# Kernel tuning notes

Hardware: AMD Instinct MI355X
Metric: run time of the kernel (lower is better)

Reference implementation:

```python
import jax, jax.numpy as jnp
import numpy as np

NUM_LAYERS = 2
FEATURES = 128
INPUT_SIZE = 128
HIDDEN = 512
BATCH = 128
SEQ_LEN = 512
PRED_LEN = 128


def _uniform(key, shape, fan):
    bound = 1.0 / np.sqrt(fan)
    return jax.random.uniform(key, shape, jnp.float32, -bound, bound)


def setup_inputs() -> dict:
    key = jax.random.key(0)
    ks = jax.random.split(key, 14)
    inp = {}
    inp["x"] = jax.random.normal(ks[0], (BATCH, SEQ_LEN, FEATURES), jnp.float32)
    # encoder Linear(features -> input_size)
    inp["enc_w"] = _uniform(ks[1], (INPUT_SIZE, FEATURES), FEATURES)
    inp["enc_b"] = _uniform(ks[2], (INPUT_SIZE,), FEATURES)
    # decoder Linear(hidden -> input_size)
    inp["dec_w"] = _uniform(ks[3], (INPUT_SIZE, HIDDEN), HIDDEN)
    inp["dec_b"] = _uniform(ks[4], (INPUT_SIZE,), HIDDEN)
    # LSTM layer 0 (input_size -> hidden), gate order i,f,g,o as in PyTorch
    inp["wih0"] = _uniform(ks[5], (4 * HIDDEN, INPUT_SIZE), HIDDEN)
    inp["whh0"] = _uniform(ks[6], (4 * HIDDEN, HIDDEN), HIDDEN)
    inp["bih0"] = _uniform(ks[7], (4 * HIDDEN,), HIDDEN)
    inp["bhh0"] = _uniform(ks[8], (4 * HIDDEN,), HIDDEN)
    # LSTM layer 1 (hidden -> hidden)
    inp["wih1"] = _uniform(ks[9], (4 * HIDDEN, HIDDEN), HIDDEN)
    inp["whh1"] = _uniform(ks[10], (4 * HIDDEN, HIDDEN), HIDDEN)
    inp["bih1"] = _uniform(ks[11], (4 * HIDDEN,), HIDDEN)
    inp["bhh1"] = _uniform(ks[12], (4 * HIDDEN,), HIDDEN)
    inp["pred_len"] = PRED_LEN
    return inp


def _lstm_cell(h, c, inp, wih, whh, bih, bhh):
    g = inp @ wih.T + bih + h @ whh.T + bhh  # [B, 4H]
    i, f, gg, o = jnp.split(g, 4, axis=-1)
    c = jax.nn.sigmoid(f) * c + jax.nn.sigmoid(i) * jnp.tanh(gg)
    h = jax.nn.sigmoid(o) * jnp.tanh(c)
    return h, c


def reference(x, enc_w, enc_b, dec_w, dec_b, wih0, whh0, bih0, bhh0,
              wih1, whh1, bih1, bhh1, pred_len):
    B, S, Fdim = x.shape
    T = S + pred_len - 1
    # pad x to T steps; beyond S the input comes from the previous output
    x_pad = jnp.concatenate([x, jnp.zeros((B, pred_len - 1, Fdim), x.dtype)], axis=1)
    x_t = jnp.transpose(x_pad, (1, 0, 2))  # [T, B, F]

    def step(carry, xs):
        h0, c0, h1, c1, prev_out = carry
        xt, t = xs
        inp = jnp.where(t < S, xt, prev_out)
        e = inp @ enc_w.T + enc_b                    # encoder
        h0, c0 = _lstm_cell(h0, c0, e, wih0, whh0, bih0, bhh0)
        h1, c1 = _lstm_cell(h1, c1, h0, wih1, whh1, bih1, bhh1)
        out = h1 @ dec_w.T + dec_b                   # decoder
        return (h0, c0, h1, c1, out), out

    z = jnp.zeros((B, HIDDEN), x.dtype)
    init = (z, z, z, z, jnp.zeros((B, Fdim), x.dtype))
    _, outs = jax.lax.scan(step, init, (x_t, jnp.arange(T)))
    # keep steps idx >= S-1 (pred_len outputs), back to [B, pred_len, input_size]
    return jnp.transpose(outs[S - 1:], (1, 0, 2))
```

## Files before the change

### kernel.cpp

```cpp
#include <hip/hip_runtime.h>
#include <math.h>

#define HID 512
#define FEAT 128
#define SEQL 512
#define PREDL 128
#define NWG 256
#define HK 516
#define EK 132

typedef float v2f __attribute__((ext_vector_type(2)));

__device__ __forceinline__ float sigf_(float x) { return 1.0f / (1.0f + __expf(-x)); }
__device__ __forceinline__ float tanh_(float x) {
  float ax = fabsf(x);
  float e2 = __expf(-2.0f * ax);
  return copysignf((1.0f - e2) / (1.0f + e2), x);
}
__device__ __forceinline__ v2f mkv2(float a, float b) { v2f r; r[0] = a; r[1] = b; return r; }

__device__ __forceinline__ void stg_sc(float* p, float v) {
  __hip_atomic_store(p, v, __ATOMIC_RELAXED, __HIP_MEMORY_SCOPE_AGENT);
}

__device__ __forceinline__ void bar_arrive(int* __restrict__ bar, int grp,
                                           int phase, int tid, bool& last) {
  __syncthreads();
  if (tid == 0) {
    const int a = __hip_atomic_fetch_add(bar + grp * 32, 1, __ATOMIC_RELAXED,
                                         __HIP_MEMORY_SCOPE_AGENT);
    last = (a == 32 * phase - 1);
    if (last)
      __hip_atomic_store(bar + 512 + grp * 32, phase, __ATOMIC_RELAXED,
                         __HIP_MEMORY_SCOPE_AGENT);
  }
  asm volatile("" ::: "memory");
}
__device__ __forceinline__ void bar_wait(int* __restrict__ bar, int grp,
                                         int phase, int tid, bool last) {
  asm volatile("" ::: "memory");
  if (tid == 0 && !last) {
    while (__hip_atomic_load(bar + 512 + grp * 32, __ATOMIC_RELAXED,
                             __HIP_MEMORY_SCOPE_AGENT) < phase)
      __builtin_amdgcn_s_sleep(1);
  }
  __syncthreads();
}

__device__ __forceinline__ void stage4(float* __restrict__ dst,
                                       const float* __restrict__ src,
                                       int b0, int lane512) {
  const int kb = lane512 >> 2;
  const int bq = (lane512 & 3) * 4;
  const float* p0 = src + (size_t)kb * 128 + b0 + bq;
  const float* p1 = src + ((size_t)kb + 128) * 128 + b0 + bq;
  const float* p2 = src + ((size_t)kb + 256) * 128 + b0 + bq;
  const float* p3 = src + ((size_t)kb + 384) * 128 + b0 + bq;
  float4 r0, r1, r2, r3;
  asm volatile(
      "global_load_dwordx4 %0, %4, off sc0 sc1\n\t"
      "global_load_dwordx4 %1, %5, off sc0 sc1\n\t"
      "global_load_dwordx4 %2, %6, off sc0 sc1\n\t"
      "global_load_dwordx4 %3, %7, off sc0 sc1\n\t"
      "s_waitcnt vmcnt(0)"
      : "=&v"(r0), "=&v"(r1), "=&v"(r2), "=&v"(r3)
      : "v"(p0), "v"(p1), "v"(p2), "v"(p3)
      : "memory");
  dst[(bq + 0) * HK + kb] = r0.x; dst[(bq + 1) * HK + kb] = r0.y;
  dst[(bq + 2) * HK + kb] = r0.z; dst[(bq + 3) * HK + kb] = r0.w;
  dst[(bq + 0) * HK + kb + 128] = r1.x; dst[(bq + 1) * HK + kb + 128] = r1.y;
  dst[(bq + 2) * HK + kb + 128] = r1.z; dst[(bq + 3) * HK + kb + 128] = r1.w;
  dst[(bq + 0) * HK + kb + 256] = r2.x; dst[(bq + 1) * HK + kb + 256] = r2.y;
  dst[(bq + 2) * HK + kb + 256] = r2.z; dst[(bq + 3) * HK + kb + 256] = r2.w;
  dst[(bq + 0) * HK + kb + 384] = r3.x; dst[(bq + 1) * HK + kb + 384] = r3.y;
  dst[(bq + 2) * HK + kb + 384] = r3.z; dst[(bq + 3) * HK + kb + 384] = r3.w;
}
__device__ __forceinline__ void stage_x1(float* __restrict__ dst,
                                         const float* __restrict__ x, int t,
                                         int b0, int lane512) {
  const int bb = lane512 >> 5;
  const int fq = (lane512 & 31) * 4;
  const float4 v =
      *(const float4*)(x + ((size_t)(b0 + bb) * SEQL + t) * FEAT + fq);
  *(float4*)(dst + bb * EK + fq) = v;
}

__device__ __forceinline__ void pkf(v2f& a01, v2f& a23, float4 w, float h) {
  v2f hh; hh[0] = h; hh[1] = h;
  v2f lo; lo[0] = w.x; lo[1] = w.y;
  v2f hi; hi[0] = w.z; hi[1] = w.w;
  a01 = __builtin_elementwise_fma(lo, hh, a01);
  a23 = __builtin_elementwise_fma(hi, hh, a23);
}
__device__ __forceinline__ void gemv_fused8(v2f& a01, v2f& a23,
                                            const float4* __restrict__ W8,
                                            size_t base,
                                            const float* __restrict__ rA,
                                            const float* __restrict__ rB,
                                            int k4b, int k4e) {
#pragma unroll 2
  for (int k4 = k4b; k4 < k4e; ++k4) {
    const float4 hA = *(const float4*)(rA + k4 * 4);
    const float4 hB = *(const float4*)(rB + k4 * 4);
    const size_t o = base + (size_t)k4 * 8;
    pkf(a01, a23, W8[o + 0], hA.x); pkf(a01, a23, W8[o + 1], hB.x);
    pkf(a01, a23, W8[o + 2], hA.y); pkf(a01, a23, W8[o + 3], hB.y);
    pkf(a01, a23, W8[o + 4], hA.z); pkf(a01, a23, W8[o + 5], hB.z);
    pkf(a01, a23, W8[o + 6], hA.w); pkf(a01, a23, W8[o + 7], hB.w);
  }
}
__device__ __forceinline__ void gemv_half8(v2f& a01, v2f& a23,
                                           const float4* __restrict__ W8,
                                           size_t base, int sel,
                                           const float* __restrict__ row,
                                           int k4b, int k4e) {
#pragma unroll 4
  for (int k4 = k4b; k4 < k4e; ++k4) {
    const float4 h = *(const float4*)(row + k4 * 4);
    const size_t o = base + (size_t)k4 * 8 + sel;
    pkf(a01, a23, W8[o + 0], h.x);
    pkf(a01, a23, W8[o + 2], h.y);
    pkf(a01, a23, W8[o + 4], h.z);
    pkf(a01, a23, W8[o + 6], h.w);
  }
}
__device__ __forceinline__ void gemv_p4(v2f& a01, v2f& a23,
                                        const float4* __restrict__ W4,
                                        size_t base,
                                        const float* __restrict__ row,
                                        int k4b, int k4e) {
#pragma unroll 4
  for (int k4 = k4b; k4 < k4e; ++k4) {
    const float4 h = *(const float4*)(row + k4 * 4);
    const size_t o = base + (size_t)k4 * 4;
    pkf(a01, a23, W4[o + 0], h.x);
    pkf(a01, a23, W4[o + 1], h.y);
    pkf(a01, a23, W4[o + 2], h.z);
    pkf(a01, a23, W4[o + 3], h.w);
  }
}

__device__ __forceinline__ void act_store(v2f a01, v2f a23, float& c_reg,
                                          float* __restrict__ HoutT,
                                          size_t cit) {
  const float ig = sigf_(a01[0]), fg = sigf_(a01[1]);
  const float gg = tanh_(a23[0]), og = sigf_(a23[1]);
  const float cn = fg * c_reg + ig * gg;
  c_reg = cn;
  stg_sc(HoutT + cit, og * tanh_(cn));
}

__global__ __launch_bounds__(1024, 1) void k_persist(
    const float* __restrict__ x,
    const float* __restrict__ enc2, const float* __restrict__ enc_b,
    const float* __restrict__ wih04, const float* __restrict__ Wa8,
    const float* __restrict__ Wf8,
    const float* __restrict__ bih0, const float* __restrict__ bhh0,
    const float* __restrict__ bih1, const float* __restrict__ bhh1,
    const float* __restrict__ dec4, const float* __restrict__ dec_b,
    const float* __restrict__ bcomp,
    float* __restrict__ h0A, float* __restrict__ h0B,
    float* __restrict__ h1A, float* __restrict__ h1B,
    int* __restrict__ bar, float* __restrict__ out) {
  __shared__ float s_h0[16 * HK];
  __shared__ float s_h1[16 * HK];
  __shared__ float s_x[16 * EK];
  __shared__ float s_e[16 * EK];
  __shared__ float4 s_red4[768];

  const int wg = blockIdx.x;
  const int tid = threadIdx.x;
  const int ut = (wg & 7) * 4 + ((wg >> 3) & 3);
  const int bt = wg >> 5;
  const int b0 = bt * 16;
  const int o = tid & 255;
  const int u = o >> 4, b = o & 15;
  const int ug = ut * 16 + u;
  const size_t cit = (size_t)ug * 128 + b0 + b;
  const int crewB = tid >> 9;
  const int khalf = (tid >> 8) & 1;
  const int lane512 = tid & 511;
  const int q4 = ((tid >> 8) + 2) & 3;

  float* h0b[2] = {h0A, h0B};
  float* h1b[2] = {h1A, h1B};
  const float* sh0row = s_h0 + b * HK;
  const float* sh1row = s_h1 + b * HK;
  const float* serow = s_e + b * EK;

  const float4* W8a = (const float4*)Wa8;
  const float4* W8f = (const float4*)Wf8;
  const float4* W4i = (const float4*)wih04;
  const size_t baseG = (size_t)ug * 1024;
  const size_t baseI = (size_t)ug * 128;

  const float bt00 = bih0[ug] + bhh0[ug];
  const float bt01 = bih0[512 + ug] + bhh0[512 + ug];
  const float bt02 = bih0[1024 + ug] + bhh0[1024 + ug];
  const float bt03 = bih0[1536 + ug] + bhh0[1536 + ug];
  const float ba00 = bt00 + bcomp[ug];
  const float ba01 = bt01 + bcomp[512 + ug];
  const float ba02 = bt02 + bcomp[1024 + ug];
  const float ba03 = bt03 + bcomp[1536 + ug];
  const float b10 = bih1[ug] + bhh1[ug];
  const float b11 = bih1[512 + ug] + bhh1[512 + ug];
  const float b12 = bih1[1024 + ug] + bhh1[1024 + ug];
  const float b13 = bih1[1536 + ug] + bhh1[1536 + ug];

  const int eb = tid & 15;
  const int f2 = tid >> 4;
  const float4* EF4 = (const float4*)enc2 + (size_t)f2 * 64;
  const float encb0 = enc_b[f2 * 2], encb1 = enc_b[f2 * 2 + 1];
  const float* sxrow = s_x + eb * EK;

  const int cb = tid & 511;
  const int jq = cb >> 4, db = cb & 15;
  const float4* D4 = (const float4*)dec4;
  const size_t baseD = (size_t)jq * 512;
  const float db0 = dec_b[jq * 4], db1 = dec_b[jq * 4 + 1];
  const float db2 = dec_b[jq * 4 + 2], db3 = dec_b[jq * 4 + 3];
  const float* dhrow = s_h1 + db * HK;

  float c_reg = 0.0f;
  int ph = 0;
  bool lastf = false;

  if (tid < 512) stage_x1(s_x, x, 0, b0, lane512);
  for (int t = 0; t < SEQL; ++t) {
    const float* h0in = h0b[(t + 1) & 1];
    float* h0out = h0b[t & 1];
    const float* h1in = h1b[t & 1];
    float* h1out = h1b[(t + 1) & 1];

    if (tid < 512) stage4(s_h0, h0in, b0, lane512);
    else stage4(s_h1, h1in, b0, lane512);
    __syncthreads();

    {
      v2f acc = mkv2(encb0, encb1);
#pragma unroll 8
      for (int k2 = 0; k2 < 64; ++k2) {
        const float4 w = EF4[k2];
        const float hv0 = sxrow[2 * k2], hv1 = sxrow[2 * k2 + 1];
        acc = __builtin_elementwise_fma(mkv2(w.x, w.y), mkv2(hv0, hv0), acc);
        acc = __builtin_elementwise_fma(mkv2(w.z, w.w), mkv2(hv1, hv1), acc);
      }
      s_e[eb * EK + f2 * 2] = acc[0];
      s_e[eb * EK + f2 * 2 + 1] = acc[1];
    }
    __syncthreads();

    v2f a01, a23;
    if (!crewB) {
      if (!khalf) {
        a01 = mkv2(bt00, bt01); a23 = mkv2(bt02, bt03);
        gemv_half8(a01, a23, W8a, baseG, 1, sh0row, 0, 80);
      } else {
        a01 = mkv2(0.f, 0.f); a23 = mkv2(0.f, 0.f);
        gemv_half8(a01, a23, W8a, baseG, 1, sh0row, 80, 128);
        gemv_p4(a01, a23, W4i, baseI, serow, 0, 32);
        s_red4[o] = make_float4(a01[0], a01[1], a23[0], a23[1]);
      }
    } else {
      if (!khalf) {
        a01 = mkv2(b10, b11); a23 = mkv2(b12, b13);
        gemv_fused8(a01, a23, W8f, baseG, sh0row, sh1row, 0, 64);
      } else {
        a01 = mkv2(0.f, 0.f); a23 = mkv2(0.f, 0.f);
        gemv_fused8(a01, a23, W8f, baseG, sh0row, sh1row, 64, 128);
        s_red4[256 + o] = make_float4(a01[0], a01[1], a23[0], a23[1]);
      }
    }
    __syncthreads();
    if (!khalf) {
      const float4 p = s_red4[(crewB ? 256 : 0) + o];
      a01[0] += p.x; a01[1] += p.y; a23[0] += p.z; a23[1] += p.w;
      if (!crewB) act_store(a01, a23, c_reg, h0out, cit);
      else if (t > 0) act_store(a01, a23, c_reg, h1out, cit);
    }
    bar_arrive(bar, bt, ++ph, tid, lastf);
    if (tid < 512 && t + 1 < SEQL) stage_x1(s_x, x, t + 1, b0, lane512);
    bar_wait(bar, bt, ph, tid, lastf);
  }

  if (tid < 512) stage4(s_h0, h0b[1], b0, lane512);
  else stage4(s_h1, h1b[0], b0, lane512);
  __syncthreads();
  {
    v2f a01, a23;
    if (q4 == 0) { a01 = mkv2(b10, b11); a23 = mkv2(b12, b13); }
    else { a01 = mkv2(0.f, 0.f); a23 = mkv2(0.f, 0.f); }
    gemv_fused8(a01, a23, W8f, baseG, sh0row, sh1row, q4 * 32, q4 * 32 + 32);
    if (q4) s_red4[(q4 - 1) * 256 + o] = make_float4(a01[0], a01[1], a23[0], a23[1]);
    __syncthreads();
    if (q4 == 0) {
      const float4 p0 = s_red4[o], p1 = s_red4[256 + o], p2 = s_red4[512 + o];
      a01[0] += p0.x + p1.x + p2.x; a01[1] += p0.y + p1.y + p2.y;
      a23[0] += p0.z + p1.z + p2.z; a23[1] += p0.w + p1.w + p2.w;
      act_store(a01, a23, c_reg, h1b[1], cit);
    }
  }
  bar_arrive(bar, bt, ++ph, tid, lastf);
  bar_wait(bar, bt, ph, tid, lastf);

  for (int t = SEQL; t < SEQL + PREDL - 1; ++t) {
    const float* h1prev = h1b[(t + 1) & 1];
    const float* h0prev = h0b[(t + 1) & 1];
    float* h0cur = h0b[t & 1];
    float* h1cur = h1b[t & 1];

    if (tid < 512) stage4(s_h1, h1prev, b0, lane512);
    else stage4(s_h0, h0prev, b0, lane512);
    __syncthreads();
    v2f a01, a23;
    if (!crewB) {
      if (!khalf) { a01 = mkv2(ba00, ba01); a23 = mkv2(ba02, ba03); }
      else { a01 = mkv2(0.f, 0.f); a23 = mkv2(0.f, 0.f); }
      gemv_fused8(a01, a23, W8a, baseG, sh1row, sh0row,
                  khalf ? 64 : 0, khalf ? 128 : 64);
      if (khalf) s_red4[o] = make_float4(a01[0], a01[1], a23[0], a23[1]);
    } else {
      v2f d01 = mkv2(db0, db1), d23 = mkv2(db2, db3);
      gemv_p4(d01, d23, D4, baseD, dhrow, 0, 128);
      *(float4*)(out + ((size_t)(b0 + db) * PREDL + (t - SEQL)) * FEAT + jq * 4) =
          make_float4(d01[0], d01[1], d23[0], d23[1]);
    }
    __syncthreads();
    if (!crewB && !khalf) {
      const float4 p = s_red4[o];
      a01[0] += p.x; a01[1] += p.y; a23[0] += p.z; a23[1] += p.w;
      act_store(a01, a23, c_reg, h0cur, cit);
    }
    bar_arrive(bar, bt, ++ph, tid, lastf);
    bar_wait(bar, bt, ph, tid, lastf);

    if (tid < 512) stage4(s_h0, h0cur, b0, lane512);
    __syncthreads();
    {
      v2f c01, c23;
      if (q4 == 0) { c01 = mkv2(b10, b11); c23 = mkv2(b12, b13); }
      else { c01 = mkv2(0.f, 0.f); c23 = mkv2(0.f, 0.f); }
      gemv_fused8(c01, c23, W8f, baseG, sh0row, sh1row, q4 * 32, q4 * 32 + 32);
      if (q4) s_red4[(q4 - 1) * 256 + o] = make_float4(c01[0], c01[1], c23[0], c23[1]);
      __syncthreads();
      if (q4 == 0) {
        const float4 p0 = s_red4[o], p1 = s_red4[256 + o], p2 = s_red4[512 + o];
        c01[0] += p0.x + p1.x + p2.x; c01[1] += p0.y + p1.y + p2.y;
        c23[0] += p0.z + p1.z + p2.z; c23[1] += p0.w + p1.w + p2.w;
        act_store(c01, c23, c_reg, h1cur, cit);
      }
    }
    bar_arrive(bar, bt, ++ph, tid, lastf);
    bar_wait(bar, bt, ph, tid, lastf);
  }

  if (tid < 512) stage4(s_h1, h1b[0], b0, lane512);
  __syncthreads();
  if (crewB) {
    v2f d01 = mkv2(db0, db1), d23 = mkv2(db2, db3);
    gemv_p4(d01, d23, D4, baseD, dhrow, 0, 128);
    *(float4*)(out + ((size_t)(b0 + db) * PREDL + (PREDL - 1)) * FEAT + jq * 4) =
        make_float4(d01[0], d01[1], d23[0], d23[1]);
  }
}

__global__ void k_b1(const float* __restrict__ enc_w,
                     const float* __restrict__ dec_w, float* __restrict__ B1) {
  const int idx = blockIdx.x * 256 + threadIdx.x;
  const int j = idx >> 9, m = idx & 511;
  float acc = 0.0f;
  for (int k = 0; k < FEAT; ++k) acc += enc_w[j * FEAT + k] * dec_w[k * HID + m];
  B1[idx] = acc;
}
__global__ void k_te(const float* __restrict__ enc_w,
                     const float* __restrict__ enc_b,
                     const float* __restrict__ dec_b, float* __restrict__ te) {
  const int j = threadIdx.x;
  float acc = enc_b[j];
  for (int k = 0; k < FEAT; ++k) acc += dec_b[k] * enc_w[j * FEAT + k];
  te[j] = acc;
}
__global__ void k_bcomp(const float* __restrict__ wih0,
                        const float* __restrict__ te, float* __restrict__ bc) {
  const int n = blockIdx.x * 256 + threadIdx.x;
  float acc = 0.0f;
  for (int j = 0; j < FEAT; ++j) acc += wih0[n * FEAT + j] * te[j];
  bc[n] = acc;
}
__global__ void k_wa8(const float* __restrict__ wih0,
                      const float* __restrict__ B1,
                      const float* __restrict__ whh0, float* __restrict__ W) {
  const int idx = blockIdx.x * 256 + threadIdx.x;
  const int uu = idx >> 9, k = idx & 511;
  float c[4];
#pragma unroll
  for (int g = 0; g < 4; ++g) {
    const float* wr = wih0 + ((size_t)(g * 512 + uu)) * FEAT;
    float acc = 0.0f;
    for (int j = 0; j < FEAT; ++j) acc += wr[j] * B1[j * HID + k];
    c[g] = acc;
  }
  float4* o = (float4*)(W + ((size_t)(uu * 512 + k)) * 8);
  o[0] = make_float4(c[0], c[1], c[2], c[3]);
  o[1] = make_float4(whh0[((size_t)uu) * 512 + k],
                     whh0[((size_t)(512 + uu)) * 512 + k],
                     whh0[((size_t)(1024 + uu)) * 512 + k],
                     whh0[((size_t)(1536 + uu)) * 512 + k]);
}
__global__ void k_wf8(const float* __restrict__ wih1,
                      const float* __restrict__ whh1, float* __restrict__ W) {
  const int idx = blockIdx.x * 256 + threadIdx.x;
  const int uu = idx >> 9, k = idx & 511;
  float4* o = (float4*)(W + ((size_t)(uu * 512 + k)) * 8);
  o[0] = make_float4(wih1[((size_t)uu) * 512 + k],
                     wih1[((size_t)(512 + uu)) * 512 + k],
                     wih1[((size_t)(1024 + uu)) * 512 + k],
                     wih1[((size_t)(1536 + uu)) * 512 + k]);
  o[1] = make_float4(whh1[((size_t)uu) * 512 + k],
                     whh1[((size_t)(512 + uu)) * 512 + k],
                     whh1[((size_t)(1024 + uu)) * 512 + k],
                     whh1[((size_t)(1536 + uu)) * 512 + k]);
}
__global__ void k_wih04(const float* __restrict__ wih0, float* __restrict__ W) {
  const int idx = blockIdx.x * 256 + threadIdx.x;
  const int uu = idx >> 7, k = idx & 127;
  float4* o = (float4*)(W + ((size_t)idx) * 4);
  o[0] = make_float4(wih0[((size_t)uu) * FEAT + k],
                     wih0[((size_t)(512 + uu)) * FEAT + k],
                     wih0[((size_t)(1024 + uu)) * FEAT + k],
                     wih0[((size_t)(1536 + uu)) * FEAT + k]);
}
__global__ void k_enc2(const float* __restrict__ enc_w, float* __restrict__ W) {
  const int idx = blockIdx.x * 256 + threadIdx.x;
  const int f2 = idx >> 7, k = idx & 127;
  W[(size_t)idx * 2 + 0] = enc_w[((size_t)(f2 * 2 + 0)) * FEAT + k];
  W[(size_t)idx * 2 + 1] = enc_w[((size_t)(f2 * 2 + 1)) * FEAT + k];
}
__global__ void k_dec4(const float* __restrict__ dec_w, float* __restrict__ W) {
  const int idx = blockIdx.x * 256 + threadIdx.x;
  const int jq = idx >> 9, k = idx & 511;
  float4* o = (float4*)(W + ((size_t)idx) * 4);
  o[0] = make_float4(dec_w[((size_t)(jq * 4 + 0)) * HID + k],
                     dec_w[((size_t)(jq * 4 + 1)) * HID + k],
                     dec_w[((size_t)(jq * 4 + 2)) * HID + k],
                     dec_w[((size_t)(jq * 4 + 3)) * HID + k]);
}

#define WS_H0A 0
#define WS_H0B 65536
#define WS_H1A 131072
#define WS_H1B 196608
#define WS_BAR 262144
#define WS_B1 263168
#define WS_TE 328704
#define WS_BCOMP 328832
#define WS_WIH04 330880
#define WS_ENC2 593024
#define WS_DEC4 609408
#define WS_WA8 674944
#define WS_WF8 2772096

extern "C" void kernel_launch(void* const* d_in, const int* in_sizes, int n_in,
                              void* d_out, int out_size, void* d_ws,
                              size_t ws_size, hipStream_t stream) {
  const float* x     = (const float*)d_in[0];
  const float* enc_w = (const float*)d_in[1];
  const float* enc_b = (const float*)d_in[2];
  const float* dec_w = (const float*)d_in[3];
  const float* dec_b = (const float*)d_in[4];
  const float* wih0  = (const float*)d_in[5];
  const float* whh0  = (const float*)d_in[6];
  const float* bih0  = (const float*)d_in[7];
  const float* bhh0  = (const float*)d_in[8];
  const float* wih1  = (const float*)d_in[9];
  const float* whh1  = (const float*)d_in[10];
  const float* bih1  = (const float*)d_in[11];
  const float* bhh1  = (const float*)d_in[12];
  float* out = (float*)d_out;

  float* ws = (float*)d_ws;
  float* h0A = ws + WS_H0A;
  float* h0B = ws + WS_H0B;
  float* h1A = ws + WS_H1A;
  float* h1B = ws + WS_H1B;
  int* bar = (int*)(ws + WS_BAR);
  float* B1 = ws + WS_B1;
  float* te = ws + WS_TE;
  float* bcomp = ws + WS_BCOMP;
  float* wih04 = ws + WS_WIH04;
  float* enc2 = ws + WS_ENC2;
  float* dec4 = ws + WS_DEC4;
  float* Wa8 = ws + WS_WA8;
  float* Wf8 = ws + WS_WF8;

  hipMemsetAsync(ws, 0, (size_t)WS_B1 * sizeof(float), stream);

  k_b1<<<256, 256, 0, stream>>>(enc_w, dec_w, B1);
  k_te<<<1, 128, 0, stream>>>(enc_w, enc_b, dec_b, te);
  k_bcomp<<<8, 256, 0, stream>>>(wih0, te, bcomp);
  k_wa8<<<1024, 256, 0, stream>>>(wih0, B1, whh0, Wa8);
  k_wf8<<<1024, 256, 0, stream>>>(wih1, whh1, Wf8);
  k_wih04<<<256, 256, 0, stream>>>(wih0, wih04);
  k_enc2<<<32, 256, 0, stream>>>(enc_w, enc2);
  k_dec4<<<64, 256, 0, stream>>>(dec_w, dec4);

  k_persist<<<NWG, 1024, 0, stream>>>(
      x, enc2, enc_b, wih04, Wa8, Wf8, bih0, bhh0, bih1, bhh1,
      dec4, dec_b, bcomp, h0A, h0B, h1A, h1B, bar, out);
}
```

Before: 41.78 ms.

## Split persistent kernel into teacher and autoregressive phases with hierarchical barrier

Splits the single persistent LSTM kernel into a teacher-forced kernel and an autoregressive kernel. The two hand off cell state through a workspace buffer. The teacher phase uses a compact packed whh0 layout instead of the half-used 8-wide fused weights, which cuts wasted weight bandwidth. The per-group barrier becomes two-level, with sub-counters of 4 and replicated release flags, to reduce atomic contention. Hidden states are now stored in per-batch-tile contiguous blocks, so staging loads are contiguous. The costs are an extra kernel launch, an extra weight-repack kernel and more workspace.

```diff
diff --git a/kernel.cpp b/kernel.cpp
--- a/kernel.cpp
+++ b/kernel.cpp
@@ -24,38 +24,51 @@
 }
 
 __device__ __forceinline__ void bar_arrive(int* __restrict__ bar, int grp,
-                                           int phase, int tid, bool& last) {
+                                           int phase, int sub, int tid,
+                                           bool& last) {
   __syncthreads();
   if (tid == 0) {
-    const int a = __hip_atomic_fetch_add(bar + grp * 32, 1, __ATOMIC_RELAXED,
-                                         __HIP_MEMORY_SCOPE_AGENT);
-    last = (a == 32 * phase - 1);
-    if (last)
-      __hip_atomic_store(bar + 512 + grp * 32, phase, __ATOMIC_RELAXED,
-                         __HIP_MEMORY_SCOPE_AGENT);
+    last = false;
+    const int a = __hip_atomic_fetch_add(bar + (grp * 8 + sub) * 32, 1,
+                                         __ATOMIC_RELAXED, __HIP_MEMORY_SCOPE_AGENT);
+    if (a == 4 * phase - 1) {
+      const int rr = __hip_atomic_fetch_add(bar + 2048 + grp * 32, 1,
+                                            __ATOMIC_RELAXED, __HIP_MEMORY_SCOPE_AGENT);
+      if (rr == 8 * phase - 1) {
+#pragma unroll
+        for (int r = 0; r < 8; ++r)
+          __hip_atomic_store(bar + 2304 + (grp * 8 + r) * 32, phase,
+                             __ATOMIC_RELAXED, __HIP_MEMORY_SCOPE_AGENT);
+        last = true;
+      }
+    }
   }
   asm volatile("" ::: "memory");
 }
 __device__ __forceinline__ void bar_wait(int* __restrict__ bar, int grp,
-                                         int phase, int tid, bool last) {
+                                         int phase, int rep, int tid,
+                                         bool last) {
   asm volatile("" ::: "memory");
   if (tid == 0 && !last) {
-    while (__hip_atomic_load(bar + 512 + grp * 32, __ATOMIC_RELAXED,
-                             __HIP_MEMORY_SCOPE_AGENT) < phase)
+    while (__hip_atomic_load(bar + 2304 + (grp * 8 + rep) * 32,
+                             __ATOMIC_RELAXED, __HIP_MEMORY_SCOPE_AGENT) < phase)
       __builtin_amdgcn_s_sleep(1);
   }
   __syncthreads();
 }
 
-__device__ __forceinline__ void stage4(float* __restrict__ dst,
-                                       const float* __restrict__ src,
-                                       int b0, int lane512) {
-  const int kb = lane512 >> 2;
-  const int bq = (lane512 & 3) * 4;
-  const float* p0 = src + (size_t)kb * 128 + b0 + bq;
-  const float* p1 = src + ((size_t)kb + 128) * 128 + b0 + bq;
-  const float* p2 = src + ((size_t)kb + 256) * 128 + b0 + bq;
-  const float* p3 = src + ((size_t)kb + 384) * 128 + b0 + bq;
+__device__ __forceinline__ void scat(float* __restrict__ dst, int idx, float4 v) {
+  const int k = idx >> 2, bq = (idx & 3) * 4;
+  dst[(bq + 0) * HK + k] = v.x;
+  dst[(bq + 1) * HK + k] = v.y;
+  dst[(bq + 2) * HK + k] = v.z;
+  dst[(bq + 3) * HK + k] = v.w;
+}
+
+__device__ __forceinline__ void stage_hd(float* __restrict__ dst,
+                                         const float* __restrict__ blk,
+                                         int lane512) {
+  const float4* s4 = (const float4*)blk + lane512;
   float4 r0, r1, r2, r3;
   asm volatile(
       "global_load_dwordx4 %0, %4, off sc0 sc1\n\t"
@@ -64,18 +77,15 @@
       "global_load_dwordx4 %3, %7, off sc0 sc1\n\t"
       "s_waitcnt vmcnt(0)"
       : "=&v"(r0), "=&v"(r1), "=&v"(r2), "=&v"(r3)
-      : "v"(p0), "v"(p1), "v"(p2), "v"(p3)
+      : "v"(s4), "v"(s4 + 512), "v"(s4 + 1024), "v"(s4 + 1536)
       : "memory");
-  dst[(bq + 0) * HK + kb] = r0.x; dst[(bq + 1) * HK + kb] = r0.y;
-  dst[(bq + 2) * HK + kb] = r0.z; dst[(bq + 3) * HK + kb] = r0.w;
-  dst[(bq + 0) * HK + kb + 128] = r1.x; dst[(bq + 1) * HK + kb + 128] = r1.y;
-  dst[(bq + 2) * HK + kb + 128] = r1.z; dst[(bq + 3) * HK + kb + 128] = r1.w;
-  dst[(bq + 0) * HK + kb + 256] = r2.x; dst[(bq + 1) * HK + kb + 256] = r2.y;
-  dst[(bq + 2) * HK + kb + 256] = r2.z; dst[(bq + 3) * HK + kb + 256] = r2.w;
-  dst[(bq + 0) * HK + kb + 384] = r3.x; dst[(bq + 1) * HK + kb + 384] = r3.y;
-  dst[(bq + 2) * HK + kb + 384] = r3.z; dst[(bq + 3) * HK + kb + 384] = r3.w;
-}
-__device__ __forceinline__ void stage_x1(float* __restrict__ dst,
+  scat(dst, lane512, r0);
+  scat(dst, lane512 + 512, r1);
+  scat(dst, lane512 + 1024, r2);
+  scat(dst, lane512 + 1536, r3);
+}
+
+__device__ __forceinline__ void stage_xx(float* __restrict__ dst,
                                          const float* __restrict__ x, int t,
                                          int b0, int lane512) {
   const int bb = lane512 >> 5;
@@ -109,21 +119,6 @@
     pkf(a01, a23, W8[o + 6], hA.w); pkf(a01, a23, W8[o + 7], hB.w);
   }
 }
-__device__ __forceinline__ void gemv_half8(v2f& a01, v2f& a23,
-                                           const float4* __restrict__ W8,
-                                           size_t base, int sel,
-                                           const float* __restrict__ row,
-                                           int k4b, int k4e) {
-#pragma unroll 4
-  for (int k4 = k4b; k4 < k4e; ++k4) {
-    const float4 h = *(const float4*)(row + k4 * 4);
-    const size_t o = base + (size_t)k4 * 8 + sel;
-    pkf(a01, a23, W8[o + 0], h.x);
-    pkf(a01, a23, W8[o + 2], h.y);
-    pkf(a01, a23, W8[o + 4], h.z);
-    pkf(a01, a23, W8[o + 6], h.w);
-  }
-}
 __device__ __forceinline__ void gemv_p4(v2f& a01, v2f& a23,
                                         const float4* __restrict__ W4,
                                         size_t base,
@@ -141,46 +136,43 @@
 }
 
 __device__ __forceinline__ void act_store(v2f a01, v2f a23, float& c_reg,
-                                          float* __restrict__ HoutT,
-                                          size_t cit) {
+                                          float* __restrict__ blk, int cit) {
   const float ig = sigf_(a01[0]), fg = sigf_(a01[1]);
   const float gg = tanh_(a23[0]), og = sigf_(a23[1]);
   const float cn = fg * c_reg + ig * gg;
   c_reg = cn;
-  stg_sc(HoutT + cit, og * tanh_(cn));
-}
-
-__global__ __launch_bounds__(1024, 1) void k_persist(
+  stg_sc(blk + cit, og * tanh_(cn));
+}
+
+__global__ __launch_bounds__(1024, 1) void k_teacher(
     const float* __restrict__ x,
     const float* __restrict__ enc2, const float* __restrict__ enc_b,
-    const float* __restrict__ wih04, const float* __restrict__ Wa8,
+    const float* __restrict__ wih04, const float* __restrict__ whh04,
     const float* __restrict__ Wf8,
     const float* __restrict__ bih0, const float* __restrict__ bhh0,
     const float* __restrict__ bih1, const float* __restrict__ bhh1,
-    const float* __restrict__ dec4, const float* __restrict__ dec_b,
-    const float* __restrict__ bcomp,
     float* __restrict__ h0A, float* __restrict__ h0B,
     float* __restrict__ h1A, float* __restrict__ h1B,
-    int* __restrict__ bar, float* __restrict__ out) {
+    float* __restrict__ cbuf, int* __restrict__ bar) {
   __shared__ float s_h0[16 * HK];
   __shared__ float s_h1[16 * HK];
   __shared__ float s_x[16 * EK];
   __shared__ float s_e[16 * EK];
-  __shared__ float4 s_red4[768];
+  __shared__ float4 s_red4[512];
 
   const int wg = blockIdx.x;
   const int tid = threadIdx.x;
   const int ut = (wg & 7) * 4 + ((wg >> 3) & 3);
   const int bt = wg >> 5;
   const int b0 = bt * 16;
+  const int rep = wg & 7;
   const int o = tid & 255;
   const int u = o >> 4, b = o & 15;
   const int ug = ut * 16 + u;
-  const size_t cit = (size_t)ug * 128 + b0 + b;
+  const int cit = ug * 16 + b;
   const int crewB = tid >> 9;
   const int khalf = (tid >> 8) & 1;
   const int lane512 = tid & 511;
-  const int q4 = ((tid >> 8) + 2) & 3;
 
   float* h0b[2] = {h0A, h0B};
   float* h1b[2] = {h1A, h1B};
@@ -188,20 +180,17 @@
   const float* sh1row = s_h1 + b * HK;
   const float* serow = s_e + b * EK;
 
-  const float4* W8a = (const float4*)Wa8;
+  const float4* W4h = (const float4*)whh04;
+  const float4* W4i = (const float4*)wih04;
   const float4* W8f = (const float4*)Wf8;
-  const float4* W4i = (const float4*)wih04;
-  const size_t baseG = (size_t)ug * 1024;
+  const size_t baseH = (size_t)ug * 512;
   const size_t baseI = (size_t)ug * 128;
+  const size_t baseF = (size_t)ug * 1024;
 
   const float bt00 = bih0[ug] + bhh0[ug];
   const float bt01 = bih0[512 + ug] + bhh0[512 + ug];
   const float bt02 = bih0[1024 + ug] + bhh0[1024 + ug];
   const float bt03 = bih0[1536 + ug] + bhh0[1536 + ug];
-  const float ba00 = bt00 + bcomp[ug];
-  const float ba01 = bt01 + bcomp[512 + ug];
-  const float ba02 = bt02 + bcomp[1024 + ug];
-  const float ba03 = bt03 + bcomp[1536 + ug];
   const float b10 = bih1[ug] + bhh1[ug];
   const float b11 = bih1[512 + ug] + bhh1[512 + ug];
   const float b12 = bih1[1024 + ug] + bhh1[1024 + ug];
@@ -213,28 +202,17 @@
   const float encb0 = enc_b[f2 * 2], encb1 = enc_b[f2 * 2 + 1];
   const float* sxrow = s_x + eb * EK;
 
-  const int cb = tid & 511;
-  const int jq = cb >> 4, db = cb & 15;
-  const float4* D4 = (const float4*)dec4;
-  const size_t baseD = (size_t)jq * 512;
-  const float db0 = dec_b[jq * 4], db1 = dec_b[jq * 4 + 1];
-  const float db2 = dec_b[jq * 4 + 2], db3 = dec_b[jq * 4 + 3];
-  const float* dhrow = s_h1 + db * HK;
-
   float c_reg = 0.0f;
   int ph = 0;
   bool lastf = false;
 
-  if (tid < 512) stage_x1(s_x, x, 0, b0, lane512);
+  if (tid < 512) stage_xx(s_x, x, 0, b0, lane512);
+  __syncthreads();
+
   for (int t = 0; t < SEQL; ++t) {
-    const float* h0in = h0b[(t + 1) & 1];
-    float* h0out = h0b[t & 1];
-    const float* h1in = h1b[t & 1];
-    float* h1out = h1b[(t + 1) & 1];
-
-    if (tid < 512) stage4(s_h0, h0in, b0, lane512);
-    else stage4(s_h1, h1in, b0, lane512);
-    __syncthreads();
+    const float* blk = ((tid < 512) ? h0b[(t + 1) & 1] : h1b[t & 1]) + bt * 8192;
+    float* dst = (tid < 512) ? s_h0 : s_h1;
+    stage_hd(dst, blk, lane512);
 
     {
       v2f acc = mkv2(encb0, encb1);
@@ -254,20 +232,20 @@
     if (!crewB) {
       if (!khalf) {
         a01 = mkv2(bt00, bt01); a23 = mkv2(bt02, bt03);
-        gemv_half8(a01, a23, W8a, baseG, 1, sh0row, 0, 80);
+        gemv_p4(a01, a23, W4h, baseH, sh0row, 0, 80);
       } else {
         a01 = mkv2(0.f, 0.f); a23 = mkv2(0.f, 0.f);
-        gemv_half8(a01, a23, W8a, baseG, 1, sh0row, 80, 128);
+        gemv_p4(a01, a23, W4h, baseH, sh0row, 80, 128);
         gemv_p4(a01, a23, W4i, baseI, serow, 0, 32);
         s_red4[o] = make_float4(a01[0], a01[1], a23[0], a23[1]);
       }
     } else {
       if (!khalf) {
         a01 = mkv2(b10, b11); a23 = mkv2(b12, b13);
-        gemv_fused8(a01, a23, W8f, baseG, sh0row, sh1row, 0, 64);
+        gemv_fused8(a01, a23, W8f, baseF, sh0row, sh1row, 0, 64);
       } else {
         a01 = mkv2(0.f, 0.f); a23 = mkv2(0.f, 0.f);
-        gemv_fused8(a01, a23, W8f, baseG, sh0row, sh1row, 64, 128);
+        gemv_fused8(a01, a23, W8f, baseF, sh0row, sh1row, 64, 128);
         s_red4[256 + o] = make_float4(a01[0], a01[1], a23[0], a23[1]);
       }
     }
@@ -275,16 +253,82 @@
     if (!khalf) {
       const float4 p = s_red4[(crewB ? 256 : 0) + o];
       a01[0] += p.x; a01[1] += p.y; a23[0] += p.z; a23[1] += p.w;
-      if (!crewB) act_store(a01, a23, c_reg, h0out, cit);
-      else if (t > 0) act_store(a01, a23, c_reg, h1out, cit);
-    }
-    bar_arrive(bar, bt, ++ph, tid, lastf);
-    if (tid < 512 && t + 1 < SEQL) stage_x1(s_x, x, t + 1, b0, lane512);
-    bar_wait(bar, bt, ph, tid, lastf);
-  }
-
-  if (tid < 512) stage4(s_h0, h0b[1], b0, lane512);
-  else stage4(s_h1, h1b[0], b0, lane512);
+      if (!crewB) act_store(a01, a23, c_reg, h0b[t & 1] + bt * 8192, cit);
+      else if (t > 0) act_store(a01, a23, c_reg, h1b[(t + 1) & 1] + bt * 8192, cit);
+    }
+    bar_arrive(bar, bt, ++ph, rep, tid, lastf);
+    if (tid < 512 && t + 1 < SEQL) stage_xx(s_x, x, t + 1, b0, lane512);
+    bar_wait(bar, bt, ph, rep, tid, lastf);
+  }
+
+  if (tid < 256) cbuf[(size_t)wg * 256 + o] = c_reg;
+  else if (tid >= 512 && tid < 768) cbuf[65536 + (size_t)wg * 256 + o] = c_reg;
+}
+
+__global__ __launch_bounds__(1024, 1) void k_ar(
+    const float* __restrict__ Wa8, const float* __restrict__ Wf8,
+    const float* __restrict__ bih0, const float* __restrict__ bhh0,
+    const float* __restrict__ bih1, const float* __restrict__ bhh1,
+    const float* __restrict__ dec4, const float* __restrict__ dec_b,
+    const float* __restrict__ bcomp,
+    float* __restrict__ h0A, float* __restrict__ h0B,
+    float* __restrict__ h1A, float* __restrict__ h1B,
+    float* __restrict__ cbuf, int* __restrict__ bar,
+    float* __restrict__ out) {
+  __shared__ float s_h0[16 * HK];
+  __shared__ float s_h1[16 * HK];
+  __shared__ float4 s_red4[768];
+
+  const int wg = blockIdx.x;
+  const int tid = threadIdx.x;
+  const int ut = (wg & 7) * 4 + ((wg >> 3) & 3);
+  const int bt = wg >> 5;
+  const int b0 = bt * 16;
+  const int rep = wg & 7;
+  const int o = tid & 255;
+  const int u = o >> 4, b = o & 15;
+  const int ug = ut * 16 + u;
+  const int cit = ug * 16 + b;
+  const int crewB = tid >> 9;
+  const int khalf = (tid >> 8) & 1;
+  const int lane512 = tid & 511;
+  const int q4 = ((tid >> 8) + 2) & 3;
+
+  float* h0b[2] = {h0A, h0B};
+  float* h1b[2] = {h1A, h1B};
+  const float* sh0row = s_h0 + b * HK;
+  const float* sh1row = s_h1 + b * HK;
+
+  const float4* W8a = (const float4*)Wa8;
+  const float4* W8f = (const float4*)Wf8;
+  const size_t baseG = (size_t)ug * 1024;
+
+  const float ba00 = bih0[ug] + bhh0[ug] + bcomp[ug];
+  const float ba01 = bih0[512 + ug] + bhh0[512 + ug] + bcomp[512 + ug];
+  const float ba02 = bih0[1024 + ug] + bhh0[1024 + ug] + bcomp[1024 + ug];
+  const float ba03 = bih0[1536 + ug] + bhh0[1536 + ug] + bcomp[1536 + ug];
+  const float b10 = bih1[ug] + bhh1[ug];
+  const float b11 = bih1[512 + ug] + bhh1[512 + ug];
+  const float b12 = bih1[1024 + ug] + bhh1[1024 + ug];
+  const float b13 = bih1[1536 + ug] + bhh1[1536 + ug];
+
+  const int cb = tid & 511;
+  const int jq = cb >> 4, db = cb & 15;
+  const float4* D4 = (const float4*)dec4;
+  const size_t baseD = (size_t)jq * 512;
+  const float db0 = dec_b[jq * 4], db1 = dec_b[jq * 4 + 1];
+  const float db2 = dec_b[jq * 4 + 2], db3 = dec_b[jq * 4 + 3];
+  const float* dhrow = s_h1 + db * HK;
+
+  float c_reg = 0.0f;
+  if (tid < 256) c_reg = cbuf[(size_t)wg * 256 + o];
+  else if (tid >= 512 && tid < 768) c_reg = cbuf[65536 + (size_t)wg * 256 + o];
+
+  int ph = 0;
+  bool lastf = false;
+
+  if (tid < 512) stage_hd(s_h0, h0b[1] + bt * 8192, lane512);
+  else stage_hd(s_h1, h1b[0] + bt * 8192, lane512);
   __syncthreads();
   {
     v2f a01, a23;
@@ -297,20 +341,15 @@
       const float4 p0 = s_red4[o], p1 = s_red4[256 + o], p2 = s_red4[512 + o];
       a01[0] += p0.x + p1.x + p2.x; a01[1] += p0.y + p1.y + p2.y;
       a23[0] += p0.z + p1.z + p2.z; a23[1] += p0.w + p1.w + p2.w;
-      act_store(a01, a23, c_reg, h1b[1], cit);
-    }
-  }
-  bar_arrive(bar, bt, ++ph, tid, lastf);
-  bar_wait(bar, bt, ph, tid, lastf);
+      act_store(a01, a23, c_reg, h1b[1] + bt * 8192, cit);
+    }
+  }
+  bar_arrive(bar, bt, ++ph, rep, tid, lastf);
+  bar_wait(bar, bt, ph, rep, tid, lastf);
 
   for (int t = SEQL; t < SEQL + PREDL - 1; ++t) {
-    const float* h1prev = h1b[(t + 1) & 1];
-    const float* h0prev = h0b[(t + 1) & 1];
-    float* h0cur = h0b[t & 1];
-    float* h1cur = h1b[t & 1];
-
-    if (tid < 512) stage4(s_h1, h1prev, b0, lane512);
-    else stage4(s_h0, h0prev, b0, lane512);
+    if (tid < 512) stage_hd(s_h1, h1b[(t + 1) & 1] + bt * 8192, lane512);
+    else stage_hd(s_h0, h0b[(t + 1) & 1] + bt * 8192, lane512);
     __syncthreads();
     v2f a01, a23;
     if (!crewB) {
@@ -329,12 +368,12 @@
     if (!crewB && !khalf) {
       const float4 p = s_red4[o];
       a01[0] += p.x; a01[1] += p.y; a23[0] += p.z; a23[1] += p.w;
-      act_store(a01, a23, c_reg, h0cur, cit);
-    }
-    bar_arrive(bar, bt, ++ph, tid, lastf);
-    bar_wait(bar, bt, ph, tid, lastf);
-
-    if (tid < 512) stage4(s_h0, h0cur, b0, lane512);
+      act_store(a01, a23, c_reg, h0b[t & 1] + bt * 8192, cit);
+    }
+    bar_arrive(bar, bt, ++ph, rep, tid, lastf);
+    bar_wait(bar, bt, ph, rep, tid, lastf);
+
+    if (tid < 512) stage_hd(s_h0, h0b[t & 1] + bt * 8192, lane512);
     __syncthreads();
     {
       v2f c01, c23;
@@ -347,14 +386,14 @@
         const float4 p0 = s_red4[o], p1 = s_red4[256 + o], p2 = s_red4[512 + o];
         c01[0] += p0.x + p1.x + p2.x; c01[1] += p0.y + p1.y + p2.y;
         c23[0] += p0.z + p1.z + p2.z; c23[1] += p0.w + p1.w + p2.w;
-        act_store(c01, c23, c_reg, h1cur, cit);
+        act_store(c01, c23, c_reg, h1b[t & 1] + bt * 8192, cit);
       }
     }
-    bar_arrive(bar, bt, ++ph, tid, lastf);
-    bar_wait(bar, bt, ph, tid, lastf);
-  }
-
-  if (tid < 512) stage4(s_h1, h1b[0], b0, lane512);
+    bar_arrive(bar, bt, ++ph, rep, tid, lastf);
+    bar_wait(bar, bt, ph, rep, tid, lastf);
+  }
+
+  if (tid < 512) stage_hd(s_h1, h1b[0] + bt * 8192, lane512);
   __syncthreads();
   if (crewB) {
     v2f d01 = mkv2(db0, db1), d23 = mkv2(db2, db3);
@@ -400,35 +439,44 @@
     for (int j = 0; j < FEAT; ++j) acc += wr[j] * B1[j * HID + k];
     c[g] = acc;
   }
-  float4* o = (float4*)(W + ((size_t)(uu * 512 + k)) * 8);
-  o[0] = make_float4(c[0], c[1], c[2], c[3]);
-  o[1] = make_float4(whh0[((size_t)uu) * 512 + k],
-                     whh0[((size_t)(512 + uu)) * 512 + k],
-                     whh0[((size_t)(1024 + uu)) * 512 + k],
-                     whh0[((size_t)(1536 + uu)) * 512 + k]);
+  float4* op = (float4*)(W + ((size_t)(uu * 512 + k)) * 8);
+  op[0] = make_float4(c[0], c[1], c[2], c[3]);
+  op[1] = make_float4(whh0[((size_t)uu) * 512 + k],
+                      whh0[((size_t)(512 + uu)) * 512 + k],
+                      whh0[((size_t)(1024 + uu)) * 512 + k],
+                      whh0[((size_t)(1536 + uu)) * 512 + k]);
 }
 __global__ void k_wf8(const float* __restrict__ wih1,
                       const float* __restrict__ whh1, float* __restrict__ W) {
   const int idx = blockIdx.x * 256 + threadIdx.x;
   const int uu = idx >> 9, k = idx & 511;
-  float4* o = (float4*)(W + ((size_t)(uu * 512 + k)) * 8);
-  o[0] = make_float4(wih1[((size_t)uu) * 512 + k],
-                     wih1[((size_t)(512 + uu)) * 512 + k],
-                     wih1[((size_t)(1024 + uu)) * 512 + k],
-                     wih1[((size_t)(1536 + uu)) * 512 + k]);
-  o[1] = make_float4(whh1[((size_t)uu) * 512 + k],
-                     whh1[((size_t)(512 + uu)) * 512 + k],
-                     whh1[((size_t)(1024 + uu)) * 512 + k],
-                     whh1[((size_t)(1536 + uu)) * 512 + k]);
+  float4* op = (float4*)(W + ((size_t)(uu * 512 + k)) * 8);
+  op[0] = make_float4(wih1[((size_t)uu) * 512 + k],
+                      wih1[((size_t)(512 + uu)) * 512 + k],
+                      wih1[((size_t)(1024 + uu)) * 512 + k],
+                      wih1[((size_t)(1536 + uu)) * 512 + k]);
+  op[1] = make_float4(whh1[((size_t)uu) * 512 + k],
+                      whh1[((size_t)(512 + uu)) * 512 + k],
+                      whh1[((size_t)(1024 + uu)) * 512 + k],
+                      whh1[((size_t)(1536 + uu)) * 512 + k]);
 }
 __global__ void k_wih04(const float* __restrict__ wih0, float* __restrict__ W) {
   const int idx = blockIdx.x * 256 + threadIdx.x;
   const int uu = idx >> 7, k = idx & 127;
-  float4* o = (float4*)(W + ((size_t)idx) * 4);
-  o[0] = make_float4(wih0[((size_t)uu) * FEAT + k],
-                     wih0[((size_t)(512 + uu)) * FEAT + k],
-                     wih0[((size_t)(1024 + uu)) * FEAT + k],
-                     wih0[((size_t)(1536 + uu)) * FEAT + k]);
+  float4* op = (float4*)(W + ((size_t)idx) * 4);
+  op[0] = make_float4(wih0[((size_t)uu) * FEAT + k],
+                      wih0[((size_t)(512 + uu)) * FEAT + k],
+                      wih0[((size_t)(1024 + uu)) * FEAT + k],
+                      wih0[((size_t)(1536 + uu)) * FEAT + k]);
+}
+__global__ void k_whh04(const float* __restrict__ whh0, float* __restrict__ W) {
+  const int idx = blockIdx.x * 256 + threadIdx.x;
+  const int uu = idx >> 9, k = idx & 511;
+  float4* op = (float4*)(W + ((size_t)idx) * 4);
+  op[0] = make_float4(whh0[((size_t)uu) * 512 + k],
+                      whh0[((size_t)(512 + uu)) * 512 + k],
+                      whh0[((size_t)(1024 + uu)) * 512 + k],
+                      whh0[((size_t)(1536 + uu)) * 512 + k]);
 }
 __global__ void k_enc2(const float* __restrict__ enc_w, float* __restrict__ W) {
   const int idx = blockIdx.x * 256 + threadIdx.x;
@@ -439,26 +487,29 @@
 __global__ void k_dec4(const float* __restrict__ dec_w, float* __restrict__ W) {
   const int idx = blockIdx.x * 256 + threadIdx.x;
   const int jq = idx >> 9, k = idx & 511;
-  float4* o = (float4*)(W + ((size_t)idx) * 4);
-  o[0] = make_float4(dec_w[((size_t)(jq * 4 + 0)) * HID + k],
-                     dec_w[((size_t)(jq * 4 + 1)) * HID + k],
-                     dec_w[((size_t)(jq * 4 + 2)) * HID + k],
-                     dec_w[((size_t)(jq * 4 + 3)) * HID + k]);
+  float4* op = (float4*)(W + ((size_t)idx) * 4);
+  op[0] = make_float4(dec_w[((size_t)(jq * 4 + 0)) * HID + k],
+                      dec_w[((size_t)(jq * 4 + 1)) * HID + k],
+                      dec_w[((size_t)(jq * 4 + 2)) * HID + k],
+                      dec_w[((size_t)(jq * 4 + 3)) * HID + k]);
 }
 
 #define WS_H0A 0
 #define WS_H0B 65536
 #define WS_H1A 131072
 #define WS_H1B 196608
-#define WS_BAR 262144
-#define WS_B1 263168
-#define WS_TE 328704
-#define WS_BCOMP 328832
-#define WS_WIH04 330880
-#define WS_ENC2 593024
-#define WS_DEC4 609408
-#define WS_WA8 674944
-#define WS_WF8 2772096
+#define WS_CBUF 262144
+#define WS_BART 393216
+#define WS_BARA 401408
+#define WS_B1 409600
+#define WS_TE 475136
+#define WS_BCOMP 475264
+#define WS_WIH04 477312
+#define WS_WHH04 739456
+#define WS_ENC2 1788032
+#define WS_DEC4 1804416
+#define WS_WA8 2066560
+#define WS_WF8 4163712
 
 extern "C" void kernel_launch(void* const* d_in, const int* in_sizes, int n_in,
                               void* d_out, int out_size, void* d_ws,
@@ -483,17 +534,21 @@
   float* h0B = ws + WS_H0B;
   float* h1A = ws + WS_H1A;
   float* h1B = ws + WS_H1B;
-  int* bar = (int*)(ws + WS_BAR);
+  float* cbuf = ws + WS_CBUF;
+  int* barT = (int*)(ws + WS_BART);
+  int* barA = (int*)(ws + WS_BARA);
   float* B1 = ws + WS_B1;
   float* te = ws + WS_TE;
   float* bcomp = ws + WS_BCOMP;
   float* wih04 = ws + WS_WIH04;
+  float* whh04 = ws + WS_WHH04;
   float* enc2 = ws + WS_ENC2;
   float* dec4 = ws + WS_DEC4;
   float* Wa8 = ws + WS_WA8;
   float* Wf8 = ws + WS_WF8;
 
-  hipMemsetAsync(ws, 0, (size_t)WS_B1 * sizeof(float), stream);
+  (void)hipMemsetAsync(ws, 0, (size_t)262144 * sizeof(float), stream);
+  (void)hipMemsetAsync(ws + WS_BART, 0, (size_t)16384 * sizeof(float), stream);
 
   k_b1<<<256, 256, 0, stream>>>(enc_w, dec_w, B1);
   k_te<<<1, 128, 0, stream>>>(enc_w, enc_b, dec_b, te);
@@ -501,10 +556,15 @@
   k_wa8<<<1024, 256, 0, stream>>>(wih0, B1, whh0, Wa8);
   k_wf8<<<1024, 256, 0, stream>>>(wih1, whh1, Wf8);
   k_wih04<<<256, 256, 0, stream>>>(wih0, wih04);
+  k_whh04<<<1024, 256, 0, stream>>>(whh0, whh04);
   k_enc2<<<32, 256, 0, stream>>>(enc_w, enc2);
   k_dec4<<<64, 256, 0, stream>>>(dec_w, dec4);
 
-  k_persist<<<NWG, 1024, 0, stream>>>(
-      x, enc2, enc_b, wih04, Wa8, Wf8, bih0, bhh0, bih1, bhh1,
-      dec4, dec_b, bcomp, h0A, h0B, h1A, h1B, bar, out);
-}
+  k_teacher<<<NWG, 1024, 0, stream>>>(
+      x, enc2, enc_b, wih04, whh04, Wf8, bih0, bhh0, bih1, bhh1,
+      h0A, h0B, h1A, h1B, cbuf, barT);
+
+  k_ar<<<NWG, 1024, 0, stream>>>(
+      Wa8, Wf8, bih0, bhh0, bih1, bhh1, dec4, dec_b, bcomp,
+      h0A, h0B, h1A, h1B, cbuf, barA, out);
+}
```

Measured after the change: 40.34 ms. 1.04x faster.
